# Performance work log

Hardware: AMD Instinct MI355X
Metric: run time of the kernel (lower is better)

## Reference

```python
import jax, jax.numpy as jnp
import numpy as np

EMBED_DIM = 2048
N_HEADS = 16
N_KV_HEADS = 4
HEAD_DIM = EMBED_DIM // N_HEADS  # 128
B, T = 8, 512


def _rope_tables(seq, dim):
    # matches RoPE.__init__: freqs repeated twice along last dim
    inv_freq = 1.0 / (10000.0 ** (jnp.arange(0, dim, 2, dtype=jnp.float32) / dim))
    t = jnp.arange(seq, dtype=jnp.float32)
    freqs = jnp.outer(t, inv_freq)          # [T, dim/2]
    emb = jnp.concatenate([freqs, freqs], axis=-1)  # [T, dim]
    return jnp.cos(emb), jnp.sin(emb)


def _apply_rope(x, cos, sin):
    # x: [B, H, T, D]; rotate-half convention
    d2 = x.shape[-1] // 2
    x1, x2 = x[..., :d2], x[..., d2:]
    x_rot = jnp.concatenate([-x2, x1], axis=-1)
    return x * cos[None, None] + x_rot * sin[None, None]


def setup_inputs() -> dict:
    key = jax.random.key(0)
    k1, k2, k3, k4, k5 = jax.random.split(key, 5)
    x = jax.random.normal(k1, (B, T, EMBED_DIM), dtype=jnp.float32)
    s = 1.0 / np.sqrt(EMBED_DIM)
    # weights stored [in, out] for y = x @ W
    wq = jax.random.normal(k2, (EMBED_DIM, EMBED_DIM), dtype=jnp.float32) * s
    wk = jax.random.normal(k3, (EMBED_DIM, HEAD_DIM * N_KV_HEADS), dtype=jnp.float32) * s
    wv = jax.random.normal(k4, (EMBED_DIM, HEAD_DIM * N_KV_HEADS), dtype=jnp.float32) * s
    wo = jax.random.normal(k5, (EMBED_DIM, EMBED_DIM), dtype=jnp.float32) * s
    # causal mask: 1 where attendable, 0 -> masked to -inf
    mask = jnp.tril(jnp.ones((T, T), dtype=bool))[None, None]  # [1,1,T,T]
    return {"x": x, "wq": wq, "wk": wk, "wv": wv, "wo": wo, "mask": mask}


def reference(x, wq, wk, wv, wo, mask):
    Bx, Tx, C = x.shape
    rep = N_HEADS // N_KV_HEADS
    q = (x @ wq).reshape(Bx, Tx, N_HEADS, HEAD_DIM).transpose(0, 2, 1, 3)      # [B,H,T,D]
    k = (x @ wk).reshape(Bx, Tx, N_KV_HEADS, HEAD_DIM).transpose(0, 2, 1, 3)   # [B,Hk,T,D]
    v = (x @ wv).reshape(Bx, Tx, N_KV_HEADS, HEAD_DIM).transpose(0, 2, 1, 3)
    cos, sin = _rope_tables(Tx, HEAD_DIM)
    q = _apply_rope(q, cos, sin)
    k = _apply_rope(k, cos, sin)
    k = jnp.repeat(k, rep, axis=1)  # GQA expand -> [B,H,T,D]
    v = jnp.repeat(v, rep, axis=1)
    scale = HEAD_DIM ** -0.5
    attn = jnp.einsum('bhtd,bhsd->bhts', q, k) * scale  # [B,H,T,T]
    attn = jnp.where(mask, attn, -jnp.inf)
    attn = jax.nn.softmax(attn, axis=-1)
    out = jnp.einsum('bhts,bhsd->bhtd', attn, v)        # [B,H,T,D]
    out = out.transpose(0, 2, 1, 3).reshape(Bx, Tx, C)
    return out @ wo
```

## Files before the change

kernel.cpp:

```cpp
#include <hip/hip_runtime.h>
#include <hip/hip_bf16.h>
#include <stdint.h>


typedef __bf16 bf16x8 __attribute__((ext_vector_type(8)));
typedef float  f32x4  __attribute__((ext_vector_type(4)));
typedef float  f4     __attribute__((ext_vector_type(4)));
typedef unsigned short u16x8 __attribute__((ext_vector_type(8)));
typedef unsigned short u16x4 __attribute__((ext_vector_type(4)));
typedef unsigned short us;

template<int V> struct Ic { static constexpr int v = V; };

__device__ __forceinline__ float bf2f(us u) {
  unsigned int x = ((unsigned int)u) << 16;
  return __builtin_bit_cast(float, x);
}
__device__ __forceinline__ us f2bf(float f) {
  unsigned int x = __builtin_bit_cast(unsigned int, f);
  unsigned int r = x + 0x7fffu + ((x >> 16) & 1u);
  return (us)(r >> 16);
}

__device__ __forceinline__ void gload16(const void* gsrc, void* ldst) {
  auto g = (const __attribute__((address_space(1))) void*)gsrc;
  auto l = (__attribute__((address_space(3))) void*)ldst;
  __builtin_amdgcn_global_load_lds(g, l, 16, 0, 0);
}

#define BAR() __builtin_amdgcn_s_barrier()
#define LGK0() do { asm volatile("s_waitcnt lgkmcnt(0)" ::: "memory"); \
                    __builtin_amdgcn_sched_barrier(0); } while (0)

template<int N> __device__ __forceinline__ void VMW() {
  if constexpr (N == 0)      asm volatile("s_waitcnt vmcnt(0)" ::: "memory");
  else if constexpr (N == 2) asm volatile("s_waitcnt vmcnt(2)" ::: "memory");
  else if constexpr (N == 3) asm volatile("s_waitcnt vmcnt(3)" ::: "memory");
  else if constexpr (N == 4) asm volatile("s_waitcnt vmcnt(4)" ::: "memory");
  else static_assert(N == 0 || N == 2 || N == 3 || N == 4, "unsupported vmcnt");
  __builtin_amdgcn_sched_barrier(0);
}

__global__ __launch_bounds__(256) void prep_kernel(
    const float* __restrict__ x, const float* __restrict__ wq,
    const float* __restrict__ wk, const float* __restrict__ wv,
    const float* __restrict__ wo, us* __restrict__ xb,
    us* __restrict__ wcat, us* __restrict__ wot,
    float* __restrict__ ct, float* __restrict__ st) {
  const int bid = blockIdx.x, tid = threadIdx.x;
  if (bid < 4096) {
    size_t idx = (size_t)bid * 256 + tid;
    const f4* p = (const f4*)(x + idx * 8);
    f4 a = p[0], b = p[1];
    u16x8 o;
#pragma unroll
    for (int e = 0; e < 4; ++e) { o[e] = f2bf(a[e]); o[4 + e] = f2bf(b[e]); }
    *(u16x8*)(xb + idx * 8) = o;
  } else if (bid < 6656) {
    __shared__ float lds[64][65];
    int lb = bid - 4096;
    int bx = lb % 80, ky = lb / 80;
    const float* src; us* dst; int N, rowOff, nb;
    if (bx < 32)      { src = wq; dst = wcat; N = 2048; rowOff = 0;    nb = bx; }
    else if (bx < 40) { src = wk; dst = wcat; N = 512;  rowOff = 2048; nb = bx - 32; }
    else if (bx < 48) { src = wv; dst = wcat; N = 512;  rowOff = 2560; nb = bx - 40; }
    else              { src = wo; dst = wot;  N = 2048; rowOff = 0;    nb = bx - 48; }
    const int n0 = nb * 64, k0 = ky * 64;
    const int c = tid & 63, rq = tid >> 6;
#pragma unroll
    for (int i = 0; i < 16; ++i) {
      int r = i * 4 + rq;
      lds[r][c] = src[(size_t)(k0 + r) * N + n0 + c];
    }
    __syncthreads();
#pragma unroll
    for (int i = 0; i < 16; ++i) {
      int nr = i * 4 + rq;
      dst[(size_t)(rowOff + n0 + nr) * 2048 + k0 + c] = f2bf(lds[c][nr]);
    }
  } else {
    int idx = (bid - 6656) * 256 + tid;
    int i = idx & 63, t = idx >> 6;
    float inv = exp2f(-(float)i * (13.287712379549449f / 64.0f));
    float ang = (float)t * inv;
    ct[idx] = cosf(ang);
    st[idx] = sinf(ang);
  }
}

__global__ void rope_k_kernel(us* __restrict__ Kh,
                              const float* __restrict__ ct, const float* __restrict__ st) {
  int idx = blockIdx.x * 256 + threadIdx.x;
  int dq = idx & 15;
  int t = (idx >> 4) & 511;
  int slot = idx >> 13;
  us* rowp = Kh + ((size_t)slot * 512 + t) * 128;
  int d0 = dq * 4;
  u16x4 x1 = *(const u16x4*)(rowp + d0);
  u16x4 x2 = *(const u16x4*)(rowp + 64 + d0);
  f4 c = *(const f4*)(ct + t * 64 + d0);
  f4 s = *(const f4*)(st + t * 64 + d0);
  u16x4 o1, o2;
#pragma unroll
  for (int e = 0; e < 4; ++e) {
    float a = bf2f(x1[e]), b = bf2f(x2[e]);
    o1[e] = f2bf(a * c[e] - b * s[e]);
    o2[e] = f2bf(b * c[e] + a * s[e]);
  }
  *(u16x4*)(rowp + d0) = o1;
  *(u16x4*)(rowp + 64 + d0) = o2;
}

__device__ __forceinline__ void gemm2_core(const us* __restrict__ A,
    const us* __restrict__ Bt, const int K, const int m0, const int n0,
    us* AT, us* BT, f32x4 (&acc)[4][4]) {
  const int tid = threadIdx.x;
  const int lane = tid & 63;
  const int wid = tid >> 6;
  const int wm = wid >> 1, wn = wid & 1;
  const int lr = lane & 15, lq = lane >> 4;
  const f32x4 zz = {0.f, 0.f, 0.f, 0.f};
#pragma unroll
  for (int i = 0; i < 4; ++i)
#pragma unroll
    for (int j = 0; j < 4; ++j) acc[i][j] = zz;

  const int KT = K >> 6;
  for (int kt = 0; kt < KT; ++kt) {
    __syncthreads();
#pragma unroll
    for (int i = 0; i < 4; ++i) {
      int c = i * 256 + tid;
      int row = c >> 3, kc = (c & 7) ^ (row & 7);
      gload16(A + (size_t)(m0 + row) * K + (kt << 6) + (kc << 3), AT + c * 8);
    }
#pragma unroll
    for (int i = 0; i < 4; ++i) {
      int c = i * 256 + tid;
      int row = c >> 3, kc = (c & 7) ^ (row & 7);
      gload16(Bt + (size_t)(n0 + row) * K + (kt << 6) + (kc << 3), BT + c * 8);
    }
    __syncthreads();
#pragma unroll
    for (int ks = 0; ks < 2; ++ks) {
      bf16x8 af[4], bfm[4];
#pragma unroll
      for (int i = 0; i < 4; ++i) {
        int R = wm * 64 + i * 16 + lr;
        af[i] = *(const bf16x8*)((const char*)AT + R * 128 +
                                 ((ks * 64 + lq * 16) ^ ((R & 7) << 4)));
      }
#pragma unroll
      for (int j = 0; j < 4; ++j) {
        int R = wn * 64 + j * 16 + lr;
        bfm[j] = *(const bf16x8*)((const char*)BT + R * 128 +
                                  ((ks * 64 + lq * 16) ^ ((R & 7) << 4)));
      }
#pragma unroll
      for (int i = 0; i < 4; ++i)
#pragma unroll
        for (int j = 0; j < 4; ++j)
          acc[i][j] = __builtin_amdgcn_mfma_f32_16x16x32_bf16(af[i], bfm[j], acc[i][j], 0, 0, 0);
    }
  }
}

__global__ __launch_bounds__(256, 4) void gemm_qkv2_kernel(const us* __restrict__ xb,
    const us* __restrict__ wcat, us* __restrict__ Qh, us* __restrict__ Kh,
    us* __restrict__ Vt) {
  __shared__ __align__(16) us AT[128 * 64];
  __shared__ __align__(16) us BT[128 * 64];
  const int bid = blockIdx.x;
  const int xcd = bid & 7, c = bid >> 3;
  const int m0 = (xcd * 4 + c / 24) << 7;
  const int n0 = (c % 24) << 7;
  f32x4 acc[4][4];
  gemm2_core(xb, wcat, 2048, m0, n0, AT, BT, acc);

  const int tid = threadIdx.x, lane = tid & 63, wid = tid >> 6;
  const int wm = wid >> 1, wn = wid & 1, lr = lane & 15, lq = lane >> 4;
#pragma unroll
  for (int i = 0; i < 4; ++i)
#pragma unroll
    for (int j = 0; j < 4; ++j) {
      int col = n0 + wn * 64 + j * 16 + lr;
#pragma unroll
      for (int r = 0; r < 4; ++r) {
        int row = m0 + wm * 64 + i * 16 + lq * 4 + r;
        int bb = row >> 9, t = row & 511;
        us val = f2bf(acc[i][j][r]);
        if (col < 2048) {
          Qh[((size_t)(bb * 16 + (col >> 7)) * 512 + t) * 128 + (col & 127)] = val;
        } else if (col < 2560) {
          int cc = col - 2048;
          Kh[((size_t)(bb * 4 + (cc >> 7)) * 512 + t) * 128 + (cc & 127)] = val;
        } else {
          int cc = col - 2560;
          Vt[((size_t)(bb * 4 + (cc >> 7)) * 128 + (cc & 127)) * 512 + t] = val;
        }
      }
    }
}

template<int BM, int BN, int WM, int WN>
__device__ __forceinline__ void gemm8_core(const us* __restrict__ A,
    const us* __restrict__ Bt, const int K, const int m0, const int n0,
    us* sm, f32x4 (&acc)[BM / (16 * WM)][BN / (16 * WN)]) {
  constexpr int MF = BM / (16 * WM), NF = BN / (16 * WN);
  constexpr int MH = MF / 2, NH = NF / 2;
  constexpr int QM = MH * 16, QN = NH * 16;
  constexpr int AHALF = (BM / 2) * 64, ABUF = BM * 64, ALDS = 2 * ABUF;
  constexpr int BHALF = (BN / 2) * 64, BBUF = BN * 64;
  constexpr int AL = BM / 128, BL = BN / 128;
  const int tid = threadIdx.x, lane = tid & 63, wid = tid >> 6;
  const int wm = wid / WN, wn = wid % WN;
  const int lr = lane & 15, lq = lane >> 4;

  const f32x4 zz = {0.f, 0.f, 0.f, 0.f};
#pragma unroll
  for (int i = 0; i < MF; ++i)
#pragma unroll
    for (int j = 0; j < NF; ++j) acc[i][j] = zz;

  bf16x8 afr[MH][2], bfr[NH][2];

  auto stageA = [&](int kt, int qd, int h) {
#pragma unroll
    for (int i = 0; i < AL; ++i) {
      int c = i * 512 + tid;
      int lrow = c >> 3;
      int grow = (lrow / QM) * (2 * QM) + h * QM + (lrow % QM);
      int kcs = (c & 7) ^ (lrow & 7);
      gload16(A + (size_t)(m0 + grow) * K + (kt << 6) + (kcs << 3),
              sm + qd * ABUF + h * AHALF + c * 8);
    }
  };
  auto stageB = [&](int kt, int qd, int h) {
#pragma unroll
    for (int i = 0; i < BL; ++i) {
      int c = i * 512 + tid;
      int lrow = c >> 3;
      int grow = (lrow / QN) * (2 * QN) + h * QN + (lrow % QN);
      int kcs = (c & 7) ^ (lrow & 7);
      gload16(Bt + (size_t)(n0 + grow) * K + (kt << 6) + (kcs << 3),
              sm + ALDS + qd * BBUF + h * BHALF + c * 8);
    }
  };
  auto lda = [&](int q, int h) {
#pragma unroll
    for (int f = 0; f < MH; ++f) {
      int R = wm * QM + f * 16 + lr;
      const char* base = (const char*)(sm + q * ABUF + h * AHALF + R * 64);
      int sw = (R & 7) << 4;
#pragma unroll
      for (int ks = 0; ks < 2; ++ks)
        afr[f][ks] = *(const bf16x8*)(base + ((ks * 64 + lq * 16) ^ sw));
    }
  };
  auto ldb = [&](int q, int h) {
#pragma unroll
    for (int g = 0; g < NH; ++g) {
      int R = wn * QN + g * 16 + lr;
      const char* base = (const char*)(sm + ALDS + q * BBUF + h * BHALF + R * 64);
      int sw = (R & 7) << 4;
#pragma unroll
      for (int ks = 0; ks < 2; ++ks)
        bfr[g][ks] = *(const bf16x8*)(base + ((ks * 64 + lq * 16) ^ sw));
    }
  };
  auto mmac = [&](auto MQ, auto NQ) {
    constexpr int mq = decltype(MQ)::v, nq = decltype(NQ)::v;
    __builtin_amdgcn_s_setprio(1);
#pragma unroll
    for (int ks = 0; ks < 2; ++ks)
#pragma unroll
      for (int f = 0; f < MH; ++f)
#pragma unroll
        for (int g = 0; g < NH; ++g)
          acc[mq * MH + f][nq * NH + g] = __builtin_amdgcn_mfma_f32_16x16x32_bf16(
              afr[f][ks], bfr[g][ks], acc[mq * MH + f][nq * NH + g], 0, 0, 0);
    __builtin_amdgcn_s_setprio(0);
  };

  stageA(0, 0, 0); stageB(0, 0, 0); stageB(0, 0, 1); stageA(0, 0, 1);
  VMW<AL + BL>(); BAR();

  const int NT = K >> 6;
  for (int kt = 0; kt < NT; ++kt) {
    const int q = kt & 1, qn = q ^ 1;
    const bool pf = (kt + 1 < NT);
    lda(q, 0); ldb(q, 0);
    if (pf) stageA(kt + 1, qn, 0);
    BAR(); LGK0(); mmac(Ic<0>{}, Ic<0>{});
    if (pf) VMW<2 * AL>(); else VMW<AL>();
    BAR();
    ldb(q, 1);
    if (pf) stageB(kt + 1, qn, 0);
    BAR(); LGK0(); mmac(Ic<0>{}, Ic<1>{});
    if (pf) VMW<AL + BL>(); else VMW<0>();
    BAR();
    lda(q, 1);
    if (pf) stageB(kt + 1, qn, 1);
    BAR(); LGK0(); mmac(Ic<1>{}, Ic<1>{});
    BAR();
    ldb(q, 0);
    if (pf) stageA(kt + 1, qn, 1);
    BAR(); LGK0(); mmac(Ic<1>{}, Ic<0>{});
    if (pf) VMW<AL + BL>();
    BAR();
  }
}

__global__ __launch_bounds__(512, 2) void gemm_out8_kernel(const us* __restrict__ Ob,
    const us* __restrict__ wot, float* __restrict__ out) {
  __shared__ __align__(16) us sm[49152];
  const int bid = blockIdx.x;
  const int xcd = bid & 7, c = bid >> 3;
  const int m0 = (xcd * 2 + (c >> 4)) << 8;
  const int n0 = (c & 15) << 7;
  f32x4 acc[8][2];
  gemm8_core<256, 128, 2, 4>(Ob, wot, 2048, m0, n0, sm, acc);

  const int tid = threadIdx.x, lane = tid & 63, wid = tid >> 6;
  const int wm = wid >> 2, wn = wid & 3, lr = lane & 15, lq = lane >> 4;
#pragma unroll
  for (int f = 0; f < 8; ++f)
#pragma unroll
    for (int g = 0; g < 2; ++g) {
      int col = n0 + wn * 32 + g * 16 + lr;
#pragma unroll
      for (int r = 0; r < 4; ++r) {
        int row = m0 + wm * 128 + f * 16 + lq * 4 + r;
        out[(size_t)row * 2048 + col] = acc[f][g][r];
      }
    }
}

__global__ __launch_bounds__(256) void attn_kernel(const us* __restrict__ Qh,
    const us* __restrict__ Kh, const us* __restrict__ Vt, us* __restrict__ Oh,
    const float* __restrict__ ct, const float* __restrict__ st) {
  __shared__ __align__(16) us Ktile[64 * 128];
  __shared__ __align__(16) us Vtile[128 * 64];
  __shared__ __align__(16) us Plds[4 * 16 * 72];
  const int tid = threadIdx.x, lane = tid & 63, w = tid >> 6;
  const int lr = lane & 15, lq = lane >> 4;
  const int bid = blockIdx.x;
  const int b = bid & 7, cc_ = bid >> 3;
  const int h = cc_ & 15, qb = 7 - (cc_ >> 4);
  const int bh = b * 16 + h, kvh = h >> 2;
  const us* Kbh = Kh + (size_t)(b * 4 + kvh) * 512 * 128;
  const us* Vbh = Vt + (size_t)(b * 4 + kvh) * 128 * 512;

  const int t_abs = qb * 64 + w * 16 + lr;
  const us* Qrow = Qh + ((size_t)bh * 512 + t_abs) * 128;
  bf16x8 qf[4];
  {
    const float* cp = ct + t_abs * 64 + (lq << 3);
    const float* sp = st + t_abs * 64 + (lq << 3);
#pragma unroll
    for (int ks = 0; ks < 2; ++ks) {
      u16x8 a = *(const u16x8*)(Qrow + ks * 32 + (lq << 3));
      u16x8 bb2 = *(const u16x8*)(Qrow + 64 + ks * 32 + (lq << 3));
      u16x8 oa, ob;
#pragma unroll
      for (int e = 0; e < 8; ++e) {
        float c = cp[ks * 32 + e], s = sp[ks * 32 + e];
        float av = bf2f(a[e]), bv = bf2f(bb2[e]);
        oa[e] = f2bf((av * c - bv * s) * 0.08838834764831845f);
        ob[e] = f2bf((bv * c + av * s) * 0.08838834764831845f);
      }
      qf[ks] = __builtin_bit_cast(bf16x8, oa);
      qf[ks + 2] = __builtin_bit_cast(bf16x8, ob);
    }
  }

  const f32x4 zz = {0.f, 0.f, 0.f, 0.f};
  f32x4 o[8];
#pragma unroll
  for (int i = 0; i < 8; ++i) o[i] = zz;
  float m[4], ll[4];
#pragma unroll
  for (int r = 0; r < 4; ++r) { m[r] = -1e30f; ll[r] = 0.f; }
  us* Pw = Plds + w * 16 * 72;

  for (int j = 0; j <= qb; ++j) {
    __syncthreads();
#pragma unroll
    for (int it = 0; it < 4; ++it) {
      int c = it * 256 + tid;
      int row = c >> 4, kc = c & 15;
      gload16(Kbh + (size_t)(j * 64 + row) * 128 + ((kc ^ (row & 7)) << 3),
              Ktile + (c << 3));
    }
#pragma unroll
    for (int it = 0; it < 4; ++it) {
      int c = it * 256 + tid;
      int row = c >> 3, tc = c & 7;
      gload16(Vbh + (size_t)row * 512 + j * 64 + ((tc ^ (row & 7)) << 3),
              Vtile + (c << 3));
    }
    __syncthreads();

    f32x4 s[4];
#pragma unroll
    for (int nb = 0; nb < 4; ++nb) s[nb] = zz;
#pragma unroll
    for (int ks = 0; ks < 4; ++ks) {
#pragma unroll
      for (int nb = 0; nb < 4; ++nb) {
        int row = nb * 16 + lr;
        bf16x8 kf = *(const bf16x8*)(Ktile + (row << 7) + (((ks * 4 + lq) ^ (row & 7)) << 3));
        s[nb] = __builtin_amdgcn_mfma_f32_16x16x32_bf16(qf[ks], kf, s[nb], 0, 0, 0);
      }
    }
    if (j == qb) {
#pragma unroll
      for (int nb = 0; nb < 4; ++nb)
#pragma unroll
        for (int r = 0; r < 4; ++r)
          if (nb * 16 + lr > w * 16 + lq * 4 + r) s[nb][r] = -1e30f;
    }

    float tm[4], alpha[4], rs[4];
#pragma unroll
    for (int r = 0; r < 4; ++r)
      tm[r] = fmaxf(fmaxf(s[0][r], s[1][r]), fmaxf(s[2][r], s[3][r]));
#pragma unroll
    for (int off = 1; off < 16; off <<= 1)
#pragma unroll
      for (int r = 0; r < 4; ++r)
        tm[r] = fmaxf(tm[r], __shfl_xor(tm[r], off, 64));
#pragma unroll
    for (int r = 0; r < 4; ++r) {
      float mn = fmaxf(m[r], tm[r]);
      alpha[r] = __expf(m[r] - mn);
      m[r] = mn;
    }
#pragma unroll
    for (int nb = 0; nb < 4; ++nb)
#pragma unroll
      for (int r = 0; r < 4; ++r)
        s[nb][r] = __expf(s[nb][r] - m[r]);
#pragma unroll
    for (int r = 0; r < 4; ++r)
      rs[r] = s[0][r] + s[1][r] + s[2][r] + s[3][r];
#pragma unroll
    for (int off = 1; off < 16; off <<= 1)
#pragma unroll
      for (int r = 0; r < 4; ++r)
        rs[r] += __shfl_xor(rs[r], off, 64);
#pragma unroll
    for (int r = 0; r < 4; ++r) ll[r] = ll[r] * alpha[r] + rs[r];
#pragma unroll
    for (int i = 0; i < 8; ++i)
#pragma unroll
      for (int r = 0; r < 4; ++r) o[i][r] *= alpha[r];

#pragma unroll
    for (int nb = 0; nb < 4; ++nb)
#pragma unroll
      for (int r = 0; r < 4; ++r)
        Pw[(lq * 4 + r) * 72 + nb * 16 + lr] = f2bf(s[nb][r]);

#pragma unroll
    for (int ks2 = 0; ks2 < 2; ++ks2) {
      bf16x8 pf = *(const bf16x8*)(Pw + lr * 72 + ks2 * 32 + (lq << 3));
#pragma unroll
      for (int nd = 0; nd < 8; ++nd) {
        int d = nd * 16 + lr;
        bf16x8 vf = *(const bf16x8*)(Vtile + (d << 6) + (((ks2 * 4 + lq) ^ (d & 7)) << 3));
        o[nd] = __builtin_amdgcn_mfma_f32_16x16x32_bf16(pf, vf, o[nd], 0, 0, 0);
      }
    }
  }

  float inv[4];
#pragma unroll
  for (int r = 0; r < 4; ++r) inv[r] = 1.0f / ll[r];
  const int rowb = b * 512 + qb * 64 + w * 16 + lq * 4;
  const int colb = h * 128 + lr;
#pragma unroll
  for (int nd = 0; nd < 8; ++nd)
#pragma unroll
    for (int r = 0; r < 4; ++r)
      Oh[(size_t)(rowb + r) * 2048 + colb + nd * 16] = f2bf(o[nd][r] * inv[r]);
}

extern "C" void kernel_launch(void* const* d_in, const int* in_sizes, int n_in,
                              void* d_out, int out_size, void* d_ws, size_t ws_size,
                              hipStream_t stream) {
  const float* x  = (const float*)d_in[0];
  const float* wq = (const float*)d_in[1];
  const float* wk = (const float*)d_in[2];
  const float* wv = (const float*)d_in[3];
  const float* wo = (const float*)d_in[4];
  float* out = (float*)d_out;
  char* ws = (char*)d_ws;

  us*    xb   = (us*)(ws);
  us*    wcat = (us*)(ws + 16777216);
  us*    wot  = (us*)(ws + 29360128);
  us*    Qh   = (us*)(ws + 37748736);
  us*    Kh   = (us*)(ws + 54525952);
  us*    Vt   = (us*)(ws + 58720256);
  us*    Oh   = (us*)(ws + 67108864);
  float* ct   = (float*)(ws + 83886080);
  float* st   = (float*)(ws + 84017152);

  prep_kernel<<<6784, 256, 0, stream>>>(x, wq, wk, wv, wo, xb, wcat, wot, ct, st);
  gemm_qkv2_kernel<<<768, 256, 0, stream>>>(xb, wcat, Qh, Kh, Vt);
  rope_k_kernel<<<1024, 256, 0, stream>>>(Kh, ct, st);
  attn_kernel<<<1024, 256, 0, stream>>>(Qh, Kh, Vt, Oh, ct, st);
  gemm_out8_kernel<<<256, 512, 0, stream>>>(Oh, wot, out);
}
```

Baseline: 150.5 us.

## Switch QKV GEMM to 256x256 pipelined core with deeper prefetch schedule

Replaces the simple single-buffered 128x128 QKV GEMM with the 8-wave ping-pong GEMM core at a 256x256 tile, launched as 192 blocks of 512 threads. It also rewrites the shared core's main loop to unroll two K-tiles per iteration and prefetch further ahead, which applies to the output projection too. This targets synchronisation stalls and the low data reuse of the old QKV kernel. The cost is that 192 blocks underfill the 256 compute units and each block needs a large shared-memory footprint.

```diff
diff --git a/kernel.cpp b/kernel.cpp
--- a/kernel.cpp
+++ b/kernel.cpp
@@ -34,10 +34,9 @@
 
 template<int N> __device__ __forceinline__ void VMW() {
   if constexpr (N == 0)      asm volatile("s_waitcnt vmcnt(0)" ::: "memory");
-  else if constexpr (N == 2) asm volatile("s_waitcnt vmcnt(2)" ::: "memory");
   else if constexpr (N == 3) asm volatile("s_waitcnt vmcnt(3)" ::: "memory");
   else if constexpr (N == 4) asm volatile("s_waitcnt vmcnt(4)" ::: "memory");
-  else static_assert(N == 0 || N == 2 || N == 3 || N == 4, "unsupported vmcnt");
+  else static_assert(N == 0 || N == 3 || N == 4, "unsupported vmcnt");
   __builtin_amdgcn_sched_barrier(0);
 }
 
@@ -111,99 +110,8 @@
   *(u16x4*)(rowp + 64 + d0) = o2;
 }
 
-__device__ __forceinline__ void gemm2_core(const us* __restrict__ A,
-    const us* __restrict__ Bt, const int K, const int m0, const int n0,
-    us* AT, us* BT, f32x4 (&acc)[4][4]) {
-  const int tid = threadIdx.x;
-  const int lane = tid & 63;
-  const int wid = tid >> 6;
-  const int wm = wid >> 1, wn = wid & 1;
-  const int lr = lane & 15, lq = lane >> 4;
-  const f32x4 zz = {0.f, 0.f, 0.f, 0.f};
-#pragma unroll
-  for (int i = 0; i < 4; ++i)
-#pragma unroll
-    for (int j = 0; j < 4; ++j) acc[i][j] = zz;
-
-  const int KT = K >> 6;
-  for (int kt = 0; kt < KT; ++kt) {
-    __syncthreads();
-#pragma unroll
-    for (int i = 0; i < 4; ++i) {
-      int c = i * 256 + tid;
-      int row = c >> 3, kc = (c & 7) ^ (row & 7);
-      gload16(A + (size_t)(m0 + row) * K + (kt << 6) + (kc << 3), AT + c * 8);
-    }
-#pragma unroll
-    for (int i = 0; i < 4; ++i) {
-      int c = i * 256 + tid;
-      int row = c >> 3, kc = (c & 7) ^ (row & 7);
-      gload16(Bt + (size_t)(n0 + row) * K + (kt << 6) + (kc << 3), BT + c * 8);
-    }
-    __syncthreads();
-#pragma unroll
-    for (int ks = 0; ks < 2; ++ks) {
-      bf16x8 af[4], bfm[4];
-#pragma unroll
-      for (int i = 0; i < 4; ++i) {
-        int R = wm * 64 + i * 16 + lr;
-        af[i] = *(const bf16x8*)((const char*)AT + R * 128 +
-                                 ((ks * 64 + lq * 16) ^ ((R & 7) << 4)));
-      }
-#pragma unroll
-      for (int j = 0; j < 4; ++j) {
-        int R = wn * 64 + j * 16 + lr;
-        bfm[j] = *(const bf16x8*)((const char*)BT + R * 128 +
-                                  ((ks * 64 + lq * 16) ^ ((R & 7) << 4)));
-      }
-#pragma unroll
-      for (int i = 0; i < 4; ++i)
-#pragma unroll
-        for (int j = 0; j < 4; ++j)
-          acc[i][j] = __builtin_amdgcn_mfma_f32_16x16x32_bf16(af[i], bfm[j], acc[i][j], 0, 0, 0);
-    }
-  }
-}
-
-__global__ __launch_bounds__(256, 4) void gemm_qkv2_kernel(const us* __restrict__ xb,
-    const us* __restrict__ wcat, us* __restrict__ Qh, us* __restrict__ Kh,
-    us* __restrict__ Vt) {
-  __shared__ __align__(16) us AT[128 * 64];
-  __shared__ __align__(16) us BT[128 * 64];
-  const int bid = blockIdx.x;
-  const int xcd = bid & 7, c = bid >> 3;
-  const int m0 = (xcd * 4 + c / 24) << 7;
-  const int n0 = (c % 24) << 7;
-  f32x4 acc[4][4];
-  gemm2_core(xb, wcat, 2048, m0, n0, AT, BT, acc);
-
-  const int tid = threadIdx.x, lane = tid & 63, wid = tid >> 6;
-  const int wm = wid >> 1, wn = wid & 1, lr = lane & 15, lq = lane >> 4;
-#pragma unroll
-  for (int i = 0; i < 4; ++i)
-#pragma unroll
-    for (int j = 0; j < 4; ++j) {
-      int col = n0 + wn * 64 + j * 16 + lr;
-#pragma unroll
-      for (int r = 0; r < 4; ++r) {
-        int row = m0 + wm * 64 + i * 16 + lq * 4 + r;
-        int bb = row >> 9, t = row & 511;
-        us val = f2bf(acc[i][j][r]);
-        if (col < 2048) {
-          Qh[((size_t)(bb * 16 + (col >> 7)) * 512 + t) * 128 + (col & 127)] = val;
-        } else if (col < 2560) {
-          int cc = col - 2048;
-          Kh[((size_t)(bb * 4 + (cc >> 7)) * 512 + t) * 128 + (cc & 127)] = val;
-        } else {
-          int cc = col - 2560;
-          Vt[((size_t)(bb * 4 + (cc >> 7)) * 128 + (cc & 127)) * 512 + t] = val;
-        }
-      }
-    }
-}
-
 template<int BM, int BN, int WM, int WN>
-__device__ __forceinline__ void gemm8_core(const us* __restrict__ A,
+__device__ __forceinline__ void gemm8v2_core(const us* __restrict__ A,
     const us* __restrict__ Bt, const int K, const int m0, const int n0,
     us* sm, f32x4 (&acc)[BM / (16 * WM)][BN / (16 * WN)]) {
   constexpr int MF = BM / (16 * WM), NF = BN / (16 * WN);
@@ -283,35 +191,81 @@
   };
 
   stageA(0, 0, 0); stageB(0, 0, 0); stageB(0, 0, 1); stageA(0, 0, 1);
+  stageA(1, 1, 0); stageB(1, 1, 1);
   VMW<AL + BL>(); BAR();
 
-  const int NT = K >> 6;
-  for (int kt = 0; kt < NT; ++kt) {
-    const int q = kt & 1, qn = q ^ 1;
-    const bool pf = (kt + 1 < NT);
-    lda(q, 0); ldb(q, 0);
-    if (pf) stageA(kt + 1, qn, 0);
-    BAR(); LGK0(); mmac(Ic<0>{}, Ic<0>{});
-    if (pf) VMW<2 * AL>(); else VMW<AL>();
-    BAR();
-    ldb(q, 1);
-    if (pf) stageB(kt + 1, qn, 0);
-    BAR(); LGK0(); mmac(Ic<0>{}, Ic<1>{});
+  const int NT = K >> 6, NI = K >> 7;
+  for (int j = 0; j < NI; ++j) {
+    const int t1 = 2 * j + 1, t2 = 2 * j + 2, t3 = 2 * j + 3;
+    const bool pf = (t2 < NT);
+    lda(0, 0); ldb(0, 0);
+    stageB(t1, 1, 0);
+    BAR(); LGK0(); mmac(Ic<0>{}, Ic<0>{}); BAR();
+    ldb(0, 1);
+    stageA(t1, 1, 1);
+    BAR(); LGK0(); mmac(Ic<0>{}, Ic<1>{}); BAR();
+    lda(0, 1);
+    if (pf) stageA(t2, 0, 0);
+    BAR(); LGK0(); mmac(Ic<1>{}, Ic<1>{}); BAR();
+    ldb(0, 0);
+    if (pf) stageB(t2, 0, 1);
+    BAR(); LGK0(); mmac(Ic<1>{}, Ic<0>{});
     if (pf) VMW<AL + BL>(); else VMW<0>();
     BAR();
-    lda(q, 1);
-    if (pf) stageB(kt + 1, qn, 1);
-    BAR(); LGK0(); mmac(Ic<1>{}, Ic<1>{});
-    BAR();
-    ldb(q, 0);
-    if (pf) stageA(kt + 1, qn, 1);
+    lda(1, 0); ldb(1, 0);
+    if (pf) stageB(t2, 0, 0);
+    BAR(); LGK0(); mmac(Ic<0>{}, Ic<0>{}); BAR();
+    ldb(1, 1);
+    if (pf) stageA(t2, 0, 1);
+    BAR(); LGK0(); mmac(Ic<0>{}, Ic<1>{}); BAR();
+    lda(1, 1);
+    if (pf) stageA(t3, 1, 0);
+    BAR(); LGK0(); mmac(Ic<1>{}, Ic<1>{}); BAR();
+    ldb(1, 0);
+    if (pf) stageB(t3, 1, 1);
     BAR(); LGK0(); mmac(Ic<1>{}, Ic<0>{});
-    if (pf) VMW<AL + BL>();
+    if (pf) VMW<AL + BL>(); else VMW<0>();
     BAR();
   }
 }
 
-__global__ __launch_bounds__(512, 2) void gemm_out8_kernel(const us* __restrict__ Ob,
+__global__ __launch_bounds__(512, 2) void gemm_qkv8v2_kernel(const us* __restrict__ xb,
+    const us* __restrict__ wcat, us* __restrict__ Qh, us* __restrict__ Kh,
+    us* __restrict__ Vt) {
+  __shared__ __align__(16) us sm[65536];
+  const int bid = blockIdx.x;
+  const int xcd = bid & 7, c = bid >> 3;
+  const int m0 = (xcd * 2 + c / 12) << 8;
+  const int n0 = (c % 12) << 8;
+  f32x4 acc[8][4];
+  gemm8v2_core<256, 256, 2, 4>(xb, wcat, 2048, m0, n0, sm, acc);
+
+  const int tid = threadIdx.x, lane = tid & 63, wid = tid >> 6;
+  const int wm = wid >> 2, wn = wid & 3, lr = lane & 15, lq = lane >> 4;
+#pragma unroll
+  for (int f = 0; f < 8; ++f)
+#pragma unroll
+    for (int g = 0; g < 4; ++g) {
+      int col = n0 + wn * 64 + g * 16 + lr;
+#pragma unroll
+      for (int r = 0; r < 4; ++r) {
+        int row = m0 + wm * 128 + f * 16 + lq * 4 + r;
+        int bb = row >> 9, t = row & 511;
+        us val = f2bf(acc[f][g][r]);
+        if (col < 2048) {
+          Qh[((size_t)(bb * 16 + (col >> 7)) * 512 + t) * 128 + (col & 127)] = val;
+        } else if (col < 2560) {
+          int cc = col - 2048;
+          Kh[((size_t)(bb * 4 + (cc >> 7)) * 512 + t) * 128 + (cc & 127)] = val;
+        } else {
+          int cc = col - 2560;
+          Vt[((size_t)(bb * 4 + (cc >> 7)) * 128 + (cc & 127)) * 512 + t] = val;
+        }
+      }
+    }
+}
+
+__global__ __launch_bounds__(512, 2) void gemm_out8v2_kernel(const us* __restrict__ Ob,
     const us* __restrict__ wot, float* __restrict__ out) {
   __shared__ __align__(16) us sm[49152];
   const int bid = blockIdx.x;
@@ -319,7 +273,7 @@
   const int m0 = (xcd * 2 + (c >> 4)) << 8;
   const int n0 = (c & 15) << 7;
   f32x4 acc[8][2];
-  gemm8_core<256, 128, 2, 4>(Ob, wot, 2048, m0, n0, sm, acc);
+  gemm8v2_core<256, 128, 2, 4>(Ob, wot, 2048, m0, n0, sm, acc);
 
   const int tid = threadIdx.x, lane = tid & 63, wid = tid >> 6;
   const int wm = wid >> 2, wn = wid & 3, lr = lane & 15, lq = lane >> 4;
@@ -508,8 +462,8 @@
   float* st   = (float*)(ws + 84017152);
 
   prep_kernel<<<6784, 256, 0, stream>>>(x, wq, wk, wv, wo, xb, wcat, wot, ct, st);
-  gemm_qkv2_kernel<<<768, 256, 0, stream>>>(xb, wcat, Qh, Kh, Vt);
+  gemm_qkv8v2_kernel<<<192, 512, 0, stream>>>(xb, wcat, Qh, Kh, Vt);
   rope_k_kernel<<<1024, 256, 0, stream>>>(Kh, ct, st);
   attn_kernel<<<1024, 256, 0, stream>>>(Qh, Kh, Vt, Oh, ct, st);
-  gemm_out8_kernel<<<256, 512, 0, stream>>>(Oh, wot, out);
-}
+  gemm_out8v2_kernel<<<256, 512, 0, stream>>>(Oh, wot, out);
+}
```

Result: slower. 169.1 us (+12.3%).
